# Performance work log

Measured on AMD Instinct MI355X. Metric: run time of the kernel, lower is better.

Reference implementation:

```python
import jax, jax.numpy as jnp
import numpy as np

NQ = 10          # num_qubits
NL = 4           # num_layers (StronglyEntanglingLayers)
DIM = 2 ** NQ    # state-vector dimension = input_linear out features
B = 4096
SEQ = 512
PRED = 96

# ---- static basis-state bookkeeping (wire 0 = most significant bit, as in PennyLane) ----

def _cnot_perm(control, target):
    s = np.arange(DIM)
    bit = (s >> (NQ - 1 - control)) & 1
    return s ^ (bit << (NQ - 1 - target))

def _layer_perms():
    # StronglyEntanglingLayers default ranges: r_l = (l % (n_wires - 1)) + 1,
    # then CNOT(i, (i+r) % n) for i = 0..n-1, applied sequentially.
    perms = []
    for l in range(NL):
        r = (l % (NQ - 1)) + 1
        comp = np.arange(DIM)
        for c in range(NQ):
            g = _cnot_perm(c, (c + r) % NQ)
            comp = comp[g]          # compose: state_new[t] = state_old[comp[t]]
        perms.append(jnp.asarray(comp))
    return perms

PERMS = _layer_perms()

_bits = (np.arange(DIM)[:, None] >> (NQ - 1 - np.arange(NQ))[None, :]) & 1
SIGNS = jnp.asarray(1.0 - 2.0 * _bits, dtype=np.float32)   # [DIM, NQ] PauliZ eigenvalues


def _rot_gates(w):
    # PennyLane Rot(phi, theta, omega) = RZ(omega) @ RY(theta) @ RZ(phi); w: [L, n, 3]
    phi, theta, omega = w[..., 0], w[..., 1], w[..., 2]
    c = jnp.cos(theta / 2)
    s = jnp.sin(theta / 2)
    ep = jnp.exp(0.5j * (phi + omega))   # e^{+i(phi+omega)/2}
    em = jnp.exp(0.5j * (phi - omega))   # e^{+i(phi-omega)/2}
    m00 = jnp.conj(ep) * c
    m01 = -em * s
    m10 = jnp.conj(em) * s
    m11 = ep * c
    return jnp.stack([jnp.stack([m00, m01], -1),
                      jnp.stack([m10, m11], -1)], -2)       # [L, n, 2, 2] complex64


def _apply_1q(psi, U, wire):
    # psi: [B, DIM] complex; apply 2x2 U on `wire`
    b = psi.shape[0]
    left = 2 ** wire
    right = 2 ** (NQ - 1 - wire)
    psi = psi.reshape(b, left, 2, right)
    psi = jnp.einsum('ba,kpaq->kpbq', U, psi)
    return psi.reshape(b, DIM)


def _circuit(psi, q_weights):
    mats = _rot_gates(q_weights)
    for l in range(NL):
        for w in range(NQ):
            psi = _apply_1q(psi, mats[l, w], w)
        psi = psi[:, PERMS[l]]          # composed CNOT ring of this layer
    return psi


def reference(x, W_in, b_in, q_weights, W_out, b_out):
    h = x @ W_in.T + b_in + 1e-6                          # input_linear, then +1e-6
    norm = jnp.linalg.norm(h, axis=-1, keepdims=True)
    psi = (h / norm).astype(jnp.complex64)                # AmplitudeEmbedding(normalize=True)
    psi = _circuit(psi, q_weights)                        # StronglyEntanglingLayers
    probs = psi.real ** 2 + psi.imag ** 2
    expvals = probs @ SIGNS                               # [B, NQ] PauliZ expvals
    return expvals @ W_out.T + b_out                      # output_linear


def setup_inputs() -> dict:
    key = jax.random.key(0)
    ks = jax.random.split(key, 6)
    x = jax.random.normal(ks[0], (B, SEQ), dtype=jnp.float32)
    W_in = jax.random.normal(ks[1], (DIM, SEQ), dtype=jnp.float32) / np.sqrt(SEQ)
    b_in = jax.random.normal(ks[2], (DIM,), dtype=jnp.float32) * 0.01
    q_weights = jax.random.uniform(ks[3], (NL, NQ, 3), dtype=jnp.float32,
                                   minval=0.0, maxval=2.0 * np.pi)
    W_out = jax.random.normal(ks[4], (PRED, NQ), dtype=jnp.float32) / np.sqrt(NQ)
    b_out = jax.random.normal(ks[5], (PRED,), dtype=jnp.float32) * 0.01
    return {"x": x, "W_in": W_in, "b_in": b_in, "q_weights": q_weights,
            "W_out": W_out, "b_out": b_out}
```

## Files before the change

### kernel.cpp

```cpp
#include <hip/hip_runtime.h>
#include <math.h>

#define DIM 1024
#define NQ 10
#define NL 4
#define SEQ 512
#define NROWS 4096
#define PRED 96

typedef unsigned short ushort_t;
typedef unsigned int uint_t;
using half8   = __attribute__((ext_vector_type(8))) _Float16;
using float4v = __attribute__((ext_vector_type(4))) float;

__device__ inline uint_t pkh(float a, float b) {
    _Float16 ha = (_Float16)a, hb = (_Float16)b;
    return (uint_t)(*(ushort_t*)&ha) | ((uint_t)(*(ushort_t*)&hb) << 16);
}

__device__ inline int permf(int s, int r) {
#pragma unroll
    for (int c = 9; c >= 0; --c) {
        int t = (c + r) % 10;
        s ^= ((s >> (9 - c)) & 1) << (9 - t);
    }
    return s;
}

__global__ __launch_bounds__(256)
void convert_x_kernel(const float* __restrict__ x, ushort_t* __restrict__ xh)
{
    int i = (blockIdx.x * 256 + threadIdx.x) * 8;
    float4 a = *(const float4*)(x + i);
    float4 b = *(const float4*)(x + i + 4);
    uint4 o;
    o.x = pkh(a.x, a.y); o.y = pkh(a.z, a.w);
    o.z = pkh(b.x, b.y); o.w = pkh(b.z, b.w);
    *(uint4*)(xh + i) = o;
}

__global__ __launch_bounds__(256)
void circuit_wave_kernel(const float* __restrict__ Wi, const float* __restrict__ b_in,
                         const float* __restrict__ qw,
                         ushort_t* __restrict__ Cjm_r, ushort_t* __restrict__ Cjm_i,
                         float* __restrict__ dr, float* __restrict__ di)
{
    __shared__ float gm[NL * NQ][8];
    __shared__ float2 scr[4 * 1024];

    const int tid = threadIdx.x;
    const int lane = tid & 63;
    const int wv = tid >> 6;
    const int jorig = blockIdx.x * 4 + wv;
    const bool valid = (jorig <= SEQ);
    const int j = valid ? jorig : SEQ;

    if (tid < NL * NQ) {
        float phi = qw[tid * 3 + 0], theta = qw[tid * 3 + 1], omega = qw[tid * 3 + 2];
        float ch = cosf(theta * 0.5f), sh = sinf(theta * 0.5f);
        float a = 0.5f * (phi + omega), b = 0.5f * (phi - omega);
        float ca = cosf(a), sa = sinf(a);
        float cb = cosf(b), sb = sinf(b);
        gm[tid][0] =  ch * ca;  gm[tid][1] = -ch * sa;
        gm[tid][2] = -sh * cb;  gm[tid][3] = -sh * sb;
        gm[tid][4] =  sh * cb;  gm[tid][5] = -sh * sb;
        gm[tid][6] =  ch * ca;  gm[tid][7] =  ch * sa;
    }
    __syncthreads();

    float2 P[16];
    if (j < SEQ) {
#pragma unroll
        for (int r = 0; r < 16; ++r)
            P[r] = make_float2(Wi[(size_t)(lane * 16 + r) * SEQ + j], 0.f);
    } else {
#pragma unroll
        for (int r = 0; r < 16; ++r)
            P[r] = make_float2(b_in[lane * 16 + r] + 1e-6f, 0.f);
    }

    float2* wscr = scr + wv * 1024;

#pragma unroll
    for (int l = 0; l < NL; ++l) {
#pragma unroll
        for (int w = 0; w < NQ; ++w) {
            const float* m = gm[l * NQ + w];
            float m00r = m[0], m00i = m[1], m01r = m[2], m01i = m[3];
            float m10r = m[4], m10i = m[5], m11r = m[6], m11i = m[7];
            if (w <= 5) {
                const int lb = 5 - w;
                const int mask = 1 << lb;
                const int myb = (lane >> lb) & 1;
                float cAr = myb ? m11r : m00r, cAi = myb ? m11i : m00i;
                float cQr = myb ? m10r : m01r, cQi = myb ? m10i : m01i;
#pragma unroll
                for (int r = 0; r < 16; ++r) {
                    float ar = P[r].x, ai = P[r].y;
                    float qr_ = __shfl_xor(ar, mask, 64);
                    float qi_ = __shfl_xor(ai, mask, 64);
                    P[r].x = cAr * ar - cAi * ai + cQr * qr_ - cQi * qi_;
                    P[r].y = cAr * ai + cAi * ar + cQr * qi_ + cQi * qr_;
                }
            } else {
                const int mk = 1 << (9 - w);
#pragma unroll
                for (int r0 = 0; r0 < 16; ++r0) {
                    if (r0 & mk) continue;
                    float2 a0 = P[r0], a1 = P[r0 | mk];
                    float2 n0, n1;
                    n0.x = m00r * a0.x - m00i * a0.y + m01r * a1.x - m01i * a1.y;
                    n0.y = m00r * a0.y + m00i * a0.x + m01r * a1.y + m01i * a1.x;
                    n1.x = m10r * a0.x - m10i * a0.y + m11r * a1.x - m11i * a1.y;
                    n1.y = m10r * a0.y + m10i * a0.x + m11r * a1.y + m11i * a1.x;
                    P[r0] = n0; P[r0 | mk] = n1;
                }
            }
        }
        const int rr = l % (NQ - 1) + 1;
#pragma unroll
        for (int r = 0; r < 16; ++r) wscr[lane * 16 + r] = P[r];
        int pl = permf(lane << 4, rr);
#pragma unroll
        for (int r = 0; r < 16; ++r) {
            int src = pl ^ permf(r, rr);
            P[r] = wscr[src];
        }
    }

    if (valid) {
        if (j < SEQ) {
            uint4 o0, o1, p0, p1;
            o0.x = pkh(P[0].x,  P[1].x);  o0.y = pkh(P[2].x,  P[3].x);
            o0.z = pkh(P[4].x,  P[5].x);  o0.w = pkh(P[6].x,  P[7].x);
            o1.x = pkh(P[8].x,  P[9].x);  o1.y = pkh(P[10].x, P[11].x);
            o1.z = pkh(P[12].x, P[13].x); o1.w = pkh(P[14].x, P[15].x);
            p0.x = pkh(P[0].y,  P[1].y);  p0.y = pkh(P[2].y,  P[3].y);
            p0.z = pkh(P[4].y,  P[5].y);  p0.w = pkh(P[6].y,  P[7].y);
            p1.x = pkh(P[8].y,  P[9].y);  p1.y = pkh(P[10].y, P[11].y);
            p1.z = pkh(P[12].y, P[13].y); p1.w = pkh(P[14].y, P[15].y);
            size_t base = (size_t)j * DIM + lane * 16;
            *(uint4*)(Cjm_r + base)     = o0;
            *(uint4*)(Cjm_r + base + 8) = o1;
            *(uint4*)(Cjm_i + base)     = p0;
            *(uint4*)(Cjm_i + base + 8) = p1;
        } else {
#pragma unroll
            for (int r = 0; r < 16; ++r) {
                dr[lane * 16 + r] = P[r].x;
                di[lane * 16 + r] = P[r].y;
            }
        }
    }
}

__global__ __launch_bounds__(256)
void transpose_c_kernel(const ushort_t* __restrict__ in_r, const ushort_t* __restrict__ in_i,
                        ushort_t* __restrict__ out_r, ushort_t* __restrict__ out_i)
{
    __shared__ ushort_t Ts[64][80];
    const int tid = threadIdx.x;
    const int j0 = blockIdx.x * 64;
    const int s0 = blockIdx.y * 64;

    for (int a = 0; a < 2; ++a) {
        const ushort_t* in = a ? in_i : in_r;
        ushort_t* out = a ? out_i : out_r;
#pragma unroll
        for (int g = 0; g < 2; ++g) {
            int G = tid + g * 256;
            int jj = G >> 3, ch = G & 7;
            uint4 v = *(const uint4*)(in + (size_t)(j0 + jj) * DIM + s0 + ch * 8);
            const ushort_t* hv = (const ushort_t*)&v;
#pragma unroll
            for (int q = 0; q < 8; ++q) Ts[ch * 8 + q][jj] = hv[q];
        }
        __syncthreads();
#pragma unroll
        for (int g = 0; g < 2; ++g) {
            int G = tid + g * 256;
            int ss = G >> 3, jc = G & 7;
            uint4 v = *(const uint4*)(&Ts[ss][jc * 8]);
            *(uint4*)(out + (size_t)(s0 + ss) * SEQ + j0 + jc * 8) = v;
        }
        __syncthreads();
    }
}

#define GBM 128
#define GBNC 64
#define GBK 32
#define LDA 40
#define LDP 65

__global__ __launch_bounds__(256)
void gemm_fused_kernel(const ushort_t* __restrict__ xh,
                       const ushort_t* __restrict__ Csm_r, const ushort_t* __restrict__ Csm_i,
                       const float* __restrict__ dr, const float* __restrict__ di,
                       float* __restrict__ part)
{
    __shared__ __align__(16) char lds[GBM * LDP * 4];
    ushort_t* Ash = (ushort_t*)lds;
    ushort_t* Bsr = Ash + GBM * LDA;
    ushort_t* Bsi = Bsr + GBNC * LDA;
    float*    Ps  = (float*)lds;
    __shared__ float drs[GBNC], dis[GBNC];

    const int tid = threadIdx.x;
    const int bm = blockIdx.x, bn = blockIdx.y;
    const int lane = tid & 63, wv = tid >> 6;
    const int n0 = bn * GBNC;

    if (tid < GBNC) { drs[tid] = dr[n0 + tid]; dis[tid] = di[n0 + tid]; }

    float4v accr[2][4], acci[2][4];
#pragma unroll
    for (int a = 0; a < 2; ++a)
#pragma unroll
        for (int b = 0; b < 4; ++b) { accr[a][b] = (float4v)0.f; acci[a][b] = (float4v)0.f; }

    const int sr = tid >> 1, ko = (tid & 1) * 16;
    const ushort_t* xa = xh + (size_t)(bm * GBM + sr) * SEQ + ko;
    const int bsel = tid >> 7;
    const int nr = (tid & 127) >> 1;
    const int bko = (tid & 1) * 16;
    const ushort_t* bsrc = (bsel ? Csm_i : Csm_r) + (size_t)(n0 + nr) * SEQ + bko;
    ushort_t* bdst = (bsel ? Bsi : Bsr) + nr * LDA + bko;

    const int fm = lane & 15, kq = (lane >> 4) * 8;
    const int wrow = wv * 32;

    for (int k0 = 0; k0 < SEQ; k0 += GBK) {
        uint4 a0 = *(const uint4*)(xa + k0);
        uint4 a1 = *(const uint4*)(xa + k0 + 8);
        *(uint4*)(Ash + sr * LDA + ko)     = a0;
        *(uint4*)(Ash + sr * LDA + ko + 8) = a1;
        uint4 b0 = *(const uint4*)(bsrc + k0);
        uint4 b1 = *(const uint4*)(bsrc + k0 + 8);
        *(uint4*)bdst       = b0;
        *(uint4*)(bdst + 8) = b1;
        __syncthreads();

        half8 ah0 = *(half8*)(Ash + (wrow + fm) * LDA + kq);
        half8 ah1 = *(half8*)(Ash + (wrow + 16 + fm) * LDA + kq);
#pragma unroll
        for (int nt = 0; nt < 4; ++nt) {
            half8 br = *(half8*)(Bsr + (nt * 16 + fm) * LDA + kq);
            half8 bi = *(half8*)(Bsi + (nt * 16 + fm) * LDA + kq);
            accr[0][nt] = __builtin_amdgcn_mfma_f32_16x16x32_f16(ah0, br, accr[0][nt], 0, 0, 0);
            accr[1][nt] = __builtin_amdgcn_mfma_f32_16x16x32_f16(ah1, br, accr[1][nt], 0, 0, 0);
            acci[0][nt] = __builtin_amdgcn_mfma_f32_16x16x32_f16(ah0, bi, acci[0][nt], 0, 0, 0);
            acci[1][nt] = __builtin_amdgcn_mfma_f32_16x16x32_f16(ah1, bi, acci[1][nt], 0, 0, 0);
        }
        __syncthreads();
    }

    const int rq = (lane >> 4) * 4;
#pragma unroll
    for (int mt = 0; mt < 2; ++mt)
#pragma unroll
        for (int nt = 0; nt < 4; ++nt) {
            float drv = drs[nt * 16 + fm], div = dis[nt * 16 + fm];
#pragma unroll
            for (int reg = 0; reg < 4; ++reg) {
                int lrow = wrow + mt * 16 + rq + reg;
                float zr = accr[mt][nt][reg] + drv;
                float zi = acci[mt][nt][reg] + div;
                Ps[lrow * LDP + nt * 16 + fm] = zr * zr + zi * zi;
            }
        }
    __syncthreads();

    {
        const int row = tid >> 1, hh = tid & 1;
        const float* pr = Ps + row * LDP + hh * 32;
        float nrm = 0.f, e0 = 0.f, e1 = 0.f, e2 = 0.f, e3 = 0.f, e4 = 0.f, e5 = 0.f;
#pragma unroll
        for (int i = 0; i < 32; ++i) {
            float p = pr[i];
            int c = hh * 32 + i;
            nrm += p;
            e0 += ((c >> 5) & 1) ? -p : p;
            e1 += ((c >> 4) & 1) ? -p : p;
            e2 += ((c >> 3) & 1) ? -p : p;
            e3 += ((c >> 2) & 1) ? -p : p;
            e4 += ((c >> 1) & 1) ? -p : p;
            e5 += (c & 1) ? -p : p;
        }
        size_t base = ((size_t)(bm * GBM + row) * 32 + (bn * 2 + hh)) * 8;
        part[base + 0] = nrm;
        part[base + 1] = e0; part[base + 2] = e1; part[base + 3] = e2;
        part[base + 4] = e3; part[base + 5] = e4; part[base + 6] = e5;
    }
}

__global__ __launch_bounds__(128)
void finalize_kernel(const float* __restrict__ part, const float* __restrict__ W_out,
                     const float* __restrict__ b_out, float* __restrict__ out)
{
    __shared__ float evf[16];
    const int row = blockIdx.x, tid = threadIdx.x;

    if (tid < 64) {
        float v[11];
        if (tid < 32) {
            const float* p = part + ((size_t)row * 32 + tid) * 8;
            float4 a = *(const float4*)p;
            float4 b = *(const float4*)(p + 4);
            float nrm = a.x;
            int bnn = tid >> 1;
            v[0] = nrm;
            v[1] = (bnn & 8) ? -nrm : nrm;
            v[2] = (bnn & 4) ? -nrm : nrm;
            v[3] = (bnn & 2) ? -nrm : nrm;
            v[4] = (bnn & 1) ? -nrm : nrm;
            v[5] = a.y; v[6] = a.z; v[7] = a.w;
            v[8] = b.x; v[9] = b.y; v[10] = b.z;
        } else {
#pragma unroll
            for (int k = 0; k < 11; ++k) v[k] = 0.f;
        }
#pragma unroll
        for (int m = 16; m; m >>= 1)
#pragma unroll
            for (int k = 0; k < 11; ++k) v[k] += __shfl_xor(v[k], m, 64);
        if (tid == 0) {
            float inv = 1.0f / v[0];
#pragma unroll
            for (int k = 0; k < 10; ++k) evf[k] = v[k + 1] * inv;
        }
    }
    __syncthreads();
    if (tid < PRED) {
        float o = b_out[tid];
#pragma unroll
        for (int k = 0; k < NQ; ++k) o = fmaf(W_out[tid * NQ + k], evf[k], o);
        out[(size_t)row * PRED + tid] = o;
    }
}

extern "C" void kernel_launch(void* const* d_in, const int* in_sizes, int n_in,
                              void* d_out, int out_size, void* d_ws, size_t ws_size,
                              hipStream_t stream) {
    const float* x     = (const float*)d_in[0];
    const float* W_in  = (const float*)d_in[1];
    const float* b_in  = (const float*)d_in[2];
    const float* qw    = (const float*)d_in[3];
    const float* W_out = (const float*)d_in[4];
    const float* b_out = (const float*)d_in[5];
    float* out = (float*)d_out;

    char* w = (char*)d_ws;
    const size_t MB = 1u << 20;
    ushort_t* xh    = (ushort_t*)w;
    ushort_t* Cjm_r = (ushort_t*)(w + 4 * MB);
    ushort_t* Cjm_i = (ushort_t*)(w + 5 * MB);
    ushort_t* Csm_r = (ushort_t*)(w + 6 * MB);
    ushort_t* Csm_i = (ushort_t*)(w + 7 * MB);
    float*    dr    = (float*)(w + 8 * MB);
    float*    di    = dr + DIM;
    float*    part  = (float*)(w + 9 * MB);

    convert_x_kernel<<<NROWS * SEQ / (256 * 8), 256, 0, stream>>>(x, xh);
    circuit_wave_kernel<<<129, 256, 0, stream>>>(W_in, b_in, qw, Cjm_r, Cjm_i, dr, di);
    transpose_c_kernel<<<dim3(SEQ / 64, DIM / 64), 256, 0, stream>>>(Cjm_r, Cjm_i, Csm_r, Csm_i);
    dim3 g2(NROWS / GBM, DIM / GBNC);
    gemm_fused_kernel<<<g2, 256, 0, stream>>>(xh, Csm_r, Csm_i, dr, di, part);
    finalize_kernel<<<NROWS, 128, 0, stream>>>(part, W_out, b_out, out);
}
```

Baseline: 126.3 us.

## Fuse all stages into one cooperative kernel with grid-wide syncs

Replaces the five separate launches (x conversion, circuit, transpose, GEMM, finalize) with a single cooperative kernel of 512 blocks separated by grid.sync barriers. The circuit stage now writes its fp16 output directly in the transposed layout using scattered 2-byte stores, and the GEMM converts fp32 x to fp16 on the fly, which removes the conversion and transpose kernels. This aims to cut launch overhead and intermediate round trips, at the cost of uncoalesced stores, only one wave per block doing circuit work, and two grid-wide barriers.

```diff
diff --git a/kernel.cpp b/kernel.cpp
--- a/kernel.cpp
+++ b/kernel.cpp
@@ -1,5 +1,8 @@
 #include <hip/hip_runtime.h>
+#include <hip/hip_cooperative_groups.h>
 #include <math.h>
+
+namespace cg = cooperative_groups;
 
 #define DIM 1024
 #define NQ 10
@@ -13,6 +16,7 @@
 using half8   = __attribute__((ext_vector_type(8))) _Float16;
 using float4v = __attribute__((ext_vector_type(4))) float;
 
+__device__ inline ushort_t f2h(float f) { _Float16 h = (_Float16)f; return *(ushort_t*)&h; }
 __device__ inline uint_t pkh(float a, float b) {
     _Float16 ha = (_Float16)a, hb = (_Float16)b;
     return (uint_t)(*(ushort_t*)&ha) | ((uint_t)(*(ushort_t*)&hb) << 16);
@@ -27,33 +31,31 @@
     return s;
 }
 
-__global__ __launch_bounds__(256)
-void convert_x_kernel(const float* __restrict__ x, ushort_t* __restrict__ xh)
+#define GBM 128
+#define GBNC 64
+#define GBK 32
+#define LDA 40
+#define LDP 65
+
+__global__ __launch_bounds__(256, 2)
+void fused_kernel(const float* __restrict__ x, const float* __restrict__ Wi,
+                  const float* __restrict__ b_in, const float* __restrict__ qw,
+                  const float* __restrict__ W_out, const float* __restrict__ b_out,
+                  ushort_t* __restrict__ Csm_r, ushort_t* __restrict__ Csm_i,
+                  float* __restrict__ dr, float* __restrict__ di,
+                  float* __restrict__ part, float* __restrict__ out)
 {
-    int i = (blockIdx.x * 256 + threadIdx.x) * 8;
-    float4 a = *(const float4*)(x + i);
-    float4 b = *(const float4*)(x + i + 4);
-    uint4 o;
-    o.x = pkh(a.x, a.y); o.y = pkh(a.z, a.w);
-    o.z = pkh(b.x, b.y); o.w = pkh(b.z, b.w);
-    *(uint4*)(xh + i) = o;
-}
-
-__global__ __launch_bounds__(256)
-void circuit_wave_kernel(const float* __restrict__ Wi, const float* __restrict__ b_in,
-                         const float* __restrict__ qw,
-                         ushort_t* __restrict__ Cjm_r, ushort_t* __restrict__ Cjm_i,
-                         float* __restrict__ dr, float* __restrict__ di)
-{
+    cg::grid_group grid = cg::this_grid();
+
+    __shared__ __align__(16) char lds[GBM * LDP * 4];
     __shared__ float gm[NL * NQ][8];
-    __shared__ float2 scr[4 * 1024];
+    __shared__ float drs[GBNC], dis[GBNC];
+    __shared__ float evf8[8][12];
 
     const int tid = threadIdx.x;
     const int lane = tid & 63;
     const int wv = tid >> 6;
-    const int jorig = blockIdx.x * 4 + wv;
-    const bool valid = (jorig <= SEQ);
-    const int j = valid ? jorig : SEQ;
+    const int blk = blockIdx.x;
 
     if (tid < NL * NQ) {
         float phi = qw[tid * 3 + 0], theta = qw[tid * 3 + 1], omega = qw[tid * 3 + 2];
@@ -68,82 +70,74 @@
     }
     __syncthreads();
 
-    float2 P[16];
-    if (j < SEQ) {
-#pragma unroll
-        for (int r = 0; r < 16; ++r)
-            P[r] = make_float2(Wi[(size_t)(lane * 16 + r) * SEQ + j], 0.f);
-    } else {
-#pragma unroll
-        for (int r = 0; r < 16; ++r)
-            P[r] = make_float2(b_in[lane * 16 + r] + 1e-6f, 0.f);
-    }
-
-    float2* wscr = scr + wv * 1024;
-
-#pragma unroll
-    for (int l = 0; l < NL; ++l) {
-#pragma unroll
-        for (int w = 0; w < NQ; ++w) {
-            const float* m = gm[l * NQ + w];
-            float m00r = m[0], m00i = m[1], m01r = m[2], m01i = m[3];
-            float m10r = m[4], m10i = m[5], m11r = m[6], m11i = m[7];
-            if (w <= 5) {
-                const int lb = 5 - w;
-                const int mask = 1 << lb;
-                const int myb = (lane >> lb) & 1;
-                float cAr = myb ? m11r : m00r, cAi = myb ? m11i : m00i;
-                float cQr = myb ? m10r : m01r, cQi = myb ? m10i : m01i;
-#pragma unroll
-                for (int r = 0; r < 16; ++r) {
-                    float ar = P[r].x, ai = P[r].y;
-                    float qr_ = __shfl_xor(ar, mask, 64);
-                    float qi_ = __shfl_xor(ai, mask, 64);
-                    P[r].x = cAr * ar - cAi * ai + cQr * qr_ - cQi * qi_;
-                    P[r].y = cAr * ai + cAi * ar + cQr * qi_ + cQi * qr_;
+    const int jcol = (wv == 0) ? blk : ((blk == 0 && wv == 1) ? SEQ : -1);
+    if (jcol >= 0) {
+        float2 P[16];
+        if (jcol < SEQ) {
+#pragma unroll
+            for (int r = 0; r < 16; ++r)
+                P[r] = make_float2(Wi[(size_t)(lane * 16 + r) * SEQ + jcol], 0.f);
+        } else {
+#pragma unroll
+            for (int r = 0; r < 16; ++r)
+                P[r] = make_float2(b_in[lane * 16 + r] + 1e-6f, 0.f);
+        }
+        float2* wscr = (float2*)lds + wv * 1024;
+
+#pragma unroll
+        for (int l = 0; l < NL; ++l) {
+#pragma unroll
+            for (int w = 0; w < NQ; ++w) {
+                const float* m = gm[l * NQ + w];
+                float m00r = m[0], m00i = m[1], m01r = m[2], m01i = m[3];
+                float m10r = m[4], m10i = m[5], m11r = m[6], m11i = m[7];
+                if (w <= 5) {
+                    const int lb = 5 - w;
+                    const int mask = 1 << lb;
+                    const int myb = (lane >> lb) & 1;
+                    float cAr = myb ? m11r : m00r, cAi = myb ? m11i : m00i;
+                    float cQr = myb ? m10r : m01r, cQi = myb ? m10i : m01i;
+#pragma unroll
+                    for (int r = 0; r < 16; ++r) {
+                        float ar = P[r].x, ai = P[r].y;
+                        float qr_ = __shfl_xor(ar, mask, 64);
+                        float qi_ = __shfl_xor(ai, mask, 64);
+                        P[r].x = cAr * ar - cAi * ai + cQr * qr_ - cQi * qi_;
+                        P[r].y = cAr * ai + cAi * ar + cQr * qi_ + cQi * qr_;
+                    }
+                } else {
+                    const int mk = 1 << (9 - w);
+#pragma unroll
+                    for (int r0 = 0; r0 < 16; ++r0) {
+                        if (r0 & mk) continue;
+                        float2 a0 = P[r0], a1 = P[r0 | mk];
+                        float2 n0, n1;
+                        n0.x = m00r * a0.x - m00i * a0.y + m01r * a1.x - m01i * a1.y;
+                        n0.y = m00r * a0.y + m00i * a0.x + m01r * a1.y + m01i * a1.x;
+                        n1.x = m10r * a0.x - m10i * a0.y + m11r * a1.x - m11i * a1.y;
+                        n1.y = m10r * a0.y + m10i * a0.x + m11r * a1.y + m11i * a1.x;
+                        P[r0] = n0; P[r0 | mk] = n1;
+                    }
                 }
-            } else {
-                const int mk = 1 << (9 - w);
-#pragma unroll
-                for (int r0 = 0; r0 < 16; ++r0) {
-                    if (r0 & mk) continue;
-                    float2 a0 = P[r0], a1 = P[r0 | mk];
-                    float2 n0, n1;
-                    n0.x = m00r * a0.x - m00i * a0.y + m01r * a1.x - m01i * a1.y;
-                    n0.y = m00r * a0.y + m00i * a0.x + m01r * a1.y + m01i * a1.x;
-                    n1.x = m10r * a0.x - m10i * a0.y + m11r * a1.x - m11i * a1.y;
-                    n1.y = m10r * a0.y + m10i * a0.x + m11r * a1.y + m11i * a1.x;
-                    P[r0] = n0; P[r0 | mk] = n1;
-                }
-            }
-        }
-        const int rr = l % (NQ - 1) + 1;
-#pragma unroll
-        for (int r = 0; r < 16; ++r) wscr[lane * 16 + r] = P[r];
-        int pl = permf(lane << 4, rr);
-#pragma unroll
-        for (int r = 0; r < 16; ++r) {
-            int src = pl ^ permf(r, rr);
-            P[r] = wscr[src];
-        }
-    }
-
-    if (valid) {
-        if (j < SEQ) {
-            uint4 o0, o1, p0, p1;
-            o0.x = pkh(P[0].x,  P[1].x);  o0.y = pkh(P[2].x,  P[3].x);
-            o0.z = pkh(P[4].x,  P[5].x);  o0.w = pkh(P[6].x,  P[7].x);
-            o1.x = pkh(P[8].x,  P[9].x);  o1.y = pkh(P[10].x, P[11].x);
-            o1.z = pkh(P[12].x, P[13].x); o1.w = pkh(P[14].x, P[15].x);
-            p0.x = pkh(P[0].y,  P[1].y);  p0.y = pkh(P[2].y,  P[3].y);
-            p0.z = pkh(P[4].y,  P[5].y);  p0.w = pkh(P[6].y,  P[7].y);
-            p1.x = pkh(P[8].y,  P[9].y);  p1.y = pkh(P[10].y, P[11].y);
-            p1.z = pkh(P[12].y, P[13].y); p1.w = pkh(P[14].y, P[15].y);
-            size_t base = (size_t)j * DIM + lane * 16;
-            *(uint4*)(Cjm_r + base)     = o0;
-            *(uint4*)(Cjm_r + base + 8) = o1;
-            *(uint4*)(Cjm_i + base)     = p0;
-            *(uint4*)(Cjm_i + base + 8) = p1;
+            }
+            const int rr = l % (NQ - 1) + 1;
+#pragma unroll
+            for (int r = 0; r < 16; ++r) wscr[lane * 16 + r] = P[r];
+            int pl = permf(lane << 4, rr);
+#pragma unroll
+            for (int r = 0; r < 16; ++r) {
+                int src = pl ^ permf(r, rr);
+                P[r] = wscr[src];
+            }
+        }
+
+        if (jcol < SEQ) {
+#pragma unroll
+            for (int r = 0; r < 16; ++r) {
+                int s = lane * 16 + r;
+                Csm_r[(size_t)s * SEQ + jcol] = f2h(P[r].x);
+                Csm_i[(size_t)s * SEQ + jcol] = f2h(P[r].y);
+            }
         } else {
 #pragma unroll
             for (int r = 0; r < 16; ++r) {
@@ -152,190 +146,144 @@
             }
         }
     }
-}
-
-__global__ __launch_bounds__(256)
-void transpose_c_kernel(const ushort_t* __restrict__ in_r, const ushort_t* __restrict__ in_i,
-                        ushort_t* __restrict__ out_r, ushort_t* __restrict__ out_i)
-{
-    __shared__ ushort_t Ts[64][80];
-    const int tid = threadIdx.x;
-    const int j0 = blockIdx.x * 64;
-    const int s0 = blockIdx.y * 64;
-
-    for (int a = 0; a < 2; ++a) {
-        const ushort_t* in = a ? in_i : in_r;
-        ushort_t* out = a ? out_i : out_r;
-#pragma unroll
-        for (int g = 0; g < 2; ++g) {
-            int G = tid + g * 256;
-            int jj = G >> 3, ch = G & 7;
-            uint4 v = *(const uint4*)(in + (size_t)(j0 + jj) * DIM + s0 + ch * 8);
-            const ushort_t* hv = (const ushort_t*)&v;
-#pragma unroll
-            for (int q = 0; q < 8; ++q) Ts[ch * 8 + q][jj] = hv[q];
+    __threadfence();
+    grid.sync();
+
+    {
+        ushort_t* Ash = (ushort_t*)lds;
+        ushort_t* Bsr = Ash + GBM * LDA;
+        ushort_t* Bsi = Bsr + GBNC * LDA;
+        float*    Ps  = (float*)lds;
+
+        const int bm = blk & 31, bn = blk >> 5;
+        const int n0 = bn * GBNC;
+
+        if (tid < GBNC) { drs[tid] = dr[n0 + tid]; dis[tid] = di[n0 + tid]; }
+
+        float4v accr[2][4], acci[2][4];
+#pragma unroll
+        for (int a = 0; a < 2; ++a)
+#pragma unroll
+            for (int b = 0; b < 4; ++b) { accr[a][b] = (float4v)0.f; acci[a][b] = (float4v)0.f; }
+
+        const int sr = tid >> 1, ko = (tid & 1) * 16;
+        const float* xa = x + (size_t)(bm * GBM + sr) * SEQ + ko;
+        const int bsel = tid >> 7;
+        const int nr = (tid & 127) >> 1;
+        const int bko = (tid & 1) * 16;
+        const ushort_t* bsrc = (bsel ? Csm_i : Csm_r) + (size_t)(n0 + nr) * SEQ + bko;
+        ushort_t* bdst = (bsel ? Bsi : Bsr) + nr * LDA + bko;
+
+        const int fm = lane & 15, kq = (lane >> 4) * 8;
+        const int wrow = wv * 32;
+
+        for (int k0 = 0; k0 < SEQ; k0 += GBK) {
+            float fv[16];
+            *(float4*)&fv[0]  = *(const float4*)(xa + k0);
+            *(float4*)&fv[4]  = *(const float4*)(xa + k0 + 4);
+            *(float4*)&fv[8]  = *(const float4*)(xa + k0 + 8);
+            *(float4*)&fv[12] = *(const float4*)(xa + k0 + 12);
+            uint_t pk[8];
+#pragma unroll
+            for (int i = 0; i < 8; ++i) pk[i] = pkh(fv[2 * i], fv[2 * i + 1]);
+            uint4 b0 = *(const uint4*)(bsrc + k0);
+            uint4 b1 = *(const uint4*)(bsrc + k0 + 8);
+            __syncthreads();
+            *(uint4*)(Ash + sr * LDA + ko)     = make_uint4(pk[0], pk[1], pk[2], pk[3]);
+            *(uint4*)(Ash + sr * LDA + ko + 8) = make_uint4(pk[4], pk[5], pk[6], pk[7]);
+            *(uint4*)bdst       = b0;
+            *(uint4*)(bdst + 8) = b1;
+            __syncthreads();
+
+            half8 ah0 = *(half8*)(Ash + (wrow + fm) * LDA + kq);
+            half8 ah1 = *(half8*)(Ash + (wrow + 16 + fm) * LDA + kq);
+#pragma unroll
+            for (int nt = 0; nt < 4; ++nt) {
+                half8 br = *(half8*)(Bsr + (nt * 16 + fm) * LDA + kq);
+                half8 bi = *(half8*)(Bsi + (nt * 16 + fm) * LDA + kq);
+                accr[0][nt] = __builtin_amdgcn_mfma_f32_16x16x32_f16(ah0, br, accr[0][nt], 0, 0, 0);
+                accr[1][nt] = __builtin_amdgcn_mfma_f32_16x16x32_f16(ah1, br, accr[1][nt], 0, 0, 0);
+                acci[0][nt] = __builtin_amdgcn_mfma_f32_16x16x32_f16(ah0, bi, acci[0][nt], 0, 0, 0);
+                acci[1][nt] = __builtin_amdgcn_mfma_f32_16x16x32_f16(ah1, bi, acci[1][nt], 0, 0, 0);
+            }
         }
         __syncthreads();
-#pragma unroll
-        for (int g = 0; g < 2; ++g) {
-            int G = tid + g * 256;
-            int ss = G >> 3, jc = G & 7;
-            uint4 v = *(const uint4*)(&Ts[ss][jc * 8]);
-            *(uint4*)(out + (size_t)(s0 + ss) * SEQ + j0 + jc * 8) = v;
-        }
+
+        const int rq = (lane >> 4) * 4;
+#pragma unroll
+        for (int mt = 0; mt < 2; ++mt)
+#pragma unroll
+            for (int nt = 0; nt < 4; ++nt) {
+                float drv = drs[nt * 16 + fm], div = dis[nt * 16 + fm];
+#pragma unroll
+                for (int reg = 0; reg < 4; ++reg) {
+                    int lrow = wrow + mt * 16 + rq + reg;
+                    float zr = accr[mt][nt][reg] + drv;
+                    float zi = acci[mt][nt][reg] + div;
+                    Ps[lrow * LDP + nt * 16 + fm] = zr * zr + zi * zi;
+                }
+            }
         __syncthreads();
-    }
-}
-
-#define GBM 128
-#define GBNC 64
-#define GBK 32
-#define LDA 40
-#define LDP 65
-
-__global__ __launch_bounds__(256)
-void gemm_fused_kernel(const ushort_t* __restrict__ xh,
-                       const ushort_t* __restrict__ Csm_r, const ushort_t* __restrict__ Csm_i,
-                       const float* __restrict__ dr, const float* __restrict__ di,
-                       float* __restrict__ part)
-{
-    __shared__ __align__(16) char lds[GBM * LDP * 4];
-    ushort_t* Ash = (ushort_t*)lds;
-    ushort_t* Bsr = Ash + GBM * LDA;
-    ushort_t* Bsi = Bsr + GBNC * LDA;
-    float*    Ps  = (float*)lds;
-    __shared__ float drs[GBNC], dis[GBNC];
-
-    const int tid = threadIdx.x;
-    const int bm = blockIdx.x, bn = blockIdx.y;
-    const int lane = tid & 63, wv = tid >> 6;
-    const int n0 = bn * GBNC;
-
-    if (tid < GBNC) { drs[tid] = dr[n0 + tid]; dis[tid] = di[n0 + tid]; }
-
-    float4v accr[2][4], acci[2][4];
-#pragma unroll
-    for (int a = 0; a < 2; ++a)
-#pragma unroll
-        for (int b = 0; b < 4; ++b) { accr[a][b] = (float4v)0.f; acci[a][b] = (float4v)0.f; }
-
-    const int sr = tid >> 1, ko = (tid & 1) * 16;
-    const ushort_t* xa = xh + (size_t)(bm * GBM + sr) * SEQ + ko;
-    const int bsel = tid >> 7;
-    const int nr = (tid & 127) >> 1;
-    const int bko = (tid & 1) * 16;
-    const ushort_t* bsrc = (bsel ? Csm_i : Csm_r) + (size_t)(n0 + nr) * SEQ + bko;
-    ushort_t* bdst = (bsel ? Bsi : Bsr) + nr * LDA + bko;
-
-    const int fm = lane & 15, kq = (lane >> 4) * 8;
-    const int wrow = wv * 32;
-
-    for (int k0 = 0; k0 < SEQ; k0 += GBK) {
-        uint4 a0 = *(const uint4*)(xa + k0);
-        uint4 a1 = *(const uint4*)(xa + k0 + 8);
-        *(uint4*)(Ash + sr * LDA + ko)     = a0;
-        *(uint4*)(Ash + sr * LDA + ko + 8) = a1;
-        uint4 b0 = *(const uint4*)(bsrc + k0);
-        uint4 b1 = *(const uint4*)(bsrc + k0 + 8);
-        *(uint4*)bdst       = b0;
-        *(uint4*)(bdst + 8) = b1;
+
+        {
+            const int row = tid >> 1, hh = tid & 1;
+            const float* pr = Ps + row * LDP + hh * 32;
+            float nrm = 0.f, e0 = 0.f, e1 = 0.f, e2 = 0.f, e3 = 0.f, e4 = 0.f, e5 = 0.f;
+#pragma unroll
+            for (int i = 0; i < 32; ++i) {
+                float p = pr[i];
+                int c = hh * 32 + i;
+                nrm += p;
+                e0 += ((c >> 5) & 1) ? -p : p;
+                e1 += ((c >> 4) & 1) ? -p : p;
+                e2 += ((c >> 3) & 1) ? -p : p;
+                e3 += ((c >> 2) & 1) ? -p : p;
+                e4 += ((c >> 1) & 1) ? -p : p;
+                e5 += (c & 1) ? -p : p;
+            }
+            size_t base = ((size_t)(bm * GBM + row) * 32 + (bn * 2 + hh)) * 8;
+            part[base + 0] = nrm;
+            part[base + 1] = e0; part[base + 2] = e1; part[base + 3] = e2;
+            part[base + 4] = e3; part[base + 5] = e4; part[base + 6] = e5;
+        }
+    }
+    __threadfence();
+    grid.sync();
+
+    {
+        const int rbase = blk * 8;
+        const int half = lane >> 5, p = lane & 31;
+        const int lrow = wv * 2 + half;
+        const float* pp = part + ((size_t)(rbase + lrow) * 32 + p) * 8;
+        float4 a = *(const float4*)pp;
+        float4 b = *(const float4*)(pp + 4);
+        float v[11];
+        float nrm = a.x;
+        int bnn = p >> 1;
+        v[0] = nrm;
+        v[1] = (bnn & 8) ? -nrm : nrm;
+        v[2] = (bnn & 4) ? -nrm : nrm;
+        v[3] = (bnn & 2) ? -nrm : nrm;
+        v[4] = (bnn & 1) ? -nrm : nrm;
+        v[5] = a.y; v[6] = a.z; v[7] = a.w;
+        v[8] = b.x; v[9] = b.y; v[10] = b.z;
+#pragma unroll
+        for (int m = 16; m; m >>= 1)
+#pragma unroll
+            for (int k = 0; k < 11; ++k) v[k] += __shfl_xor(v[k], m, 64);
+        if (p == 0) {
+            float inv = 1.0f / v[0];
+#pragma unroll
+            for (int k = 0; k < 10; ++k) evf8[lrow][k] = v[k + 1] * inv;
+        }
         __syncthreads();
-
-        half8 ah0 = *(half8*)(Ash + (wrow + fm) * LDA + kq);
-        half8 ah1 = *(half8*)(Ash + (wrow + 16 + fm) * LDA + kq);
-#pragma unroll
-        for (int nt = 0; nt < 4; ++nt) {
-            half8 br = *(half8*)(Bsr + (nt * 16 + fm) * LDA + kq);
-            half8 bi = *(half8*)(Bsi + (nt * 16 + fm) * LDA + kq);
-            accr[0][nt] = __builtin_amdgcn_mfma_f32_16x16x32_f16(ah0, br, accr[0][nt], 0, 0, 0);
-            accr[1][nt] = __builtin_amdgcn_mfma_f32_16x16x32_f16(ah1, br, accr[1][nt], 0, 0, 0);
-            acci[0][nt] = __builtin_amdgcn_mfma_f32_16x16x32_f16(ah0, bi, acci[0][nt], 0, 0, 0);
-            acci[1][nt] = __builtin_amdgcn_mfma_f32_16x16x32_f16(ah1, bi, acci[1][nt], 0, 0, 0);
-        }
-        __syncthreads();
-    }
-
-    const int rq = (lane >> 4) * 4;
-#pragma unroll
-    for (int mt = 0; mt < 2; ++mt)
-#pragma unroll
-        for (int nt = 0; nt < 4; ++nt) {
-            float drv = drs[nt * 16 + fm], div = dis[nt * 16 + fm];
-#pragma unroll
-            for (int reg = 0; reg < 4; ++reg) {
-                int lrow = wrow + mt * 16 + rq + reg;
-                float zr = accr[mt][nt][reg] + drv;
-                float zi = acci[mt][nt][reg] + div;
-                Ps[lrow * LDP + nt * 16 + fm] = zr * zr + zi * zi;
-            }
-        }
-    __syncthreads();
-
-    {
-        const int row = tid >> 1, hh = tid & 1;
-        const float* pr = Ps + row * LDP + hh * 32;
-        float nrm = 0.f, e0 = 0.f, e1 = 0.f, e2 = 0.f, e3 = 0.f, e4 = 0.f, e5 = 0.f;
-#pragma unroll
-        for (int i = 0; i < 32; ++i) {
-            float p = pr[i];
-            int c = hh * 32 + i;
-            nrm += p;
-            e0 += ((c >> 5) & 1) ? -p : p;
-            e1 += ((c >> 4) & 1) ? -p : p;
-            e2 += ((c >> 3) & 1) ? -p : p;
-            e3 += ((c >> 2) & 1) ? -p : p;
-            e4 += ((c >> 1) & 1) ? -p : p;
-            e5 += (c & 1) ? -p : p;
-        }
-        size_t base = ((size_t)(bm * GBM + row) * 32 + (bn * 2 + hh)) * 8;
-        part[base + 0] = nrm;
-        part[base + 1] = e0; part[base + 2] = e1; part[base + 3] = e2;
-        part[base + 4] = e3; part[base + 5] = e4; part[base + 6] = e5;
-    }
-}
-
-__global__ __launch_bounds__(128)
-void finalize_kernel(const float* __restrict__ part, const float* __restrict__ W_out,
-                     const float* __restrict__ b_out, float* __restrict__ out)
-{
-    __shared__ float evf[16];
-    const int row = blockIdx.x, tid = threadIdx.x;
-
-    if (tid < 64) {
-        float v[11];
-        if (tid < 32) {
-            const float* p = part + ((size_t)row * 32 + tid) * 8;
-            float4 a = *(const float4*)p;
-            float4 b = *(const float4*)(p + 4);
-            float nrm = a.x;
-            int bnn = tid >> 1;
-            v[0] = nrm;
-            v[1] = (bnn & 8) ? -nrm : nrm;
-            v[2] = (bnn & 4) ? -nrm : nrm;
-            v[3] = (bnn & 2) ? -nrm : nrm;
-            v[4] = (bnn & 1) ? -nrm : nrm;
-            v[5] = a.y; v[6] = a.z; v[7] = a.w;
-            v[8] = b.x; v[9] = b.y; v[10] = b.z;
-        } else {
-#pragma unroll
-            for (int k = 0; k < 11; ++k) v[k] = 0.f;
-        }
-#pragma unroll
-        for (int m = 16; m; m >>= 1)
-#pragma unroll
-            for (int k = 0; k < 11; ++k) v[k] += __shfl_xor(v[k], m, 64);
-        if (tid == 0) {
-            float inv = 1.0f / v[0];
-#pragma unroll
-            for (int k = 0; k < 10; ++k) evf[k] = v[k + 1] * inv;
-        }
-    }
-    __syncthreads();
-    if (tid < PRED) {
-        float o = b_out[tid];
-#pragma unroll
-        for (int k = 0; k < NQ; ++k) o = fmaf(W_out[tid * NQ + k], evf[k], o);
-        out[(size_t)row * PRED + tid] = o;
+        for (int t = tid; t < 8 * PRED; t += 256) {
+            int rr = t / PRED, c = t - rr * PRED;
+            float o = b_out[c];
+#pragma unroll
+            for (int k = 0; k < NQ; ++k) o = fmaf(W_out[c * NQ + k], evf8[rr][k], o);
+            out[(size_t)(rbase + rr) * PRED + c] = o;
+        }
     }
 }
 
@@ -352,19 +300,16 @@
 
     char* w = (char*)d_ws;
     const size_t MB = 1u << 20;
-    ushort_t* xh    = (ushort_t*)w;
-    ushort_t* Cjm_r = (ushort_t*)(w + 4 * MB);
-    ushort_t* Cjm_i = (ushort_t*)(w + 5 * MB);
-    ushort_t* Csm_r = (ushort_t*)(w + 6 * MB);
-    ushort_t* Csm_i = (ushort_t*)(w + 7 * MB);
-    float*    dr    = (float*)(w + 8 * MB);
+    ushort_t* Csm_r = (ushort_t*)w;
+    ushort_t* Csm_i = (ushort_t*)(w + 1 * MB);
+    float*    dr    = (float*)(w + 2 * MB);
     float*    di    = dr + DIM;
-    float*    part  = (float*)(w + 9 * MB);
-
-    convert_x_kernel<<<NROWS * SEQ / (256 * 8), 256, 0, stream>>>(x, xh);
-    circuit_wave_kernel<<<129, 256, 0, stream>>>(W_in, b_in, qw, Cjm_r, Cjm_i, dr, di);
-    transpose_c_kernel<<<dim3(SEQ / 64, DIM / 64), 256, 0, stream>>>(Cjm_r, Cjm_i, Csm_r, Csm_i);
-    dim3 g2(NROWS / GBM, DIM / GBNC);
-    gemm_fused_kernel<<<g2, 256, 0, stream>>>(xh, Csm_r, Csm_i, dr, di, part);
-    finalize_kernel<<<NROWS, 128, 0, stream>>>(part, W_out, b_out, out);
+    float*    part  = (float*)(w + 3 * MB);
+
+    void* args[] = {(void*)&x, (void*)&W_in, (void*)&b_in, (void*)&qw,
+                    (void*)&W_out, (void*)&b_out,
+                    (void*)&Csm_r, (void*)&Csm_i, (void*)&dr, (void*)&di,
+                    (void*)&part, (void*)&out};
+    hipLaunchCooperativeKernel((void*)fused_kernel, dim3(512), dim3(256),
+                               args, 0, stream);
 }
```

Result: slower. 372.9 us (+195.2%).
